# Kernel optimization log

Hardware: AMD Instinct MI355X
Metric: run time of the kernel (lower is better)

Reference implementation:

```python
import jax, jax.numpy as jnp
import numpy as np

D_MODEL = 1024
NUM_HEADS = 16
HEAD_DIM = D_MODEL // NUM_HEADS


def setup_inputs() -> dict:
    key = jax.random.key(0)
    ks = jax.random.split(key, 5)
    s = 1.0 / np.sqrt(D_MODEL)
    return {
        "x": jax.random.normal(ks[0], (4, 2048, D_MODEL), dtype=jnp.float32),
        "w_qkv": jax.random.uniform(ks[1], (3 * D_MODEL, D_MODEL), jnp.float32, -s, s),
        "b_qkv": jax.random.uniform(ks[2], (3 * D_MODEL,), jnp.float32, -s, s),
        "w_out": jax.random.uniform(ks[3], (D_MODEL, D_MODEL), jnp.float32, -s, s),
        "b_out": jax.random.uniform(ks[4], (D_MODEL,), jnp.float32, -s, s),
    }


def reference(x, w_qkv, b_qkv, w_out, b_out):
    B, T, D = x.shape
    # torch Linear: y = x @ W^T + b
    qkv = x @ w_qkv.T + b_qkv                                  # [B,T,3D]
    qkv = qkv.reshape(B, T, 3, NUM_HEADS, HEAD_DIM)
    q, k, v = jnp.moveaxis(qkv, 2, 0)                          # each [B,T,H,Hd]
    q = q.transpose(0, 2, 1, 3)                                # [B,H,T,Hd]
    k = k.transpose(0, 2, 1, 3)
    v = v.transpose(0, 2, 1, 3)
    scale = 1.0 / np.sqrt(HEAD_DIM).astype(np.float32)
    scores = jnp.einsum("bhqd,bhkd->bhqk", q, k) * scale       # [B,H,T,T]
    attn = jax.nn.softmax(scores, axis=-1)
    out = jnp.einsum("bhqk,bhkd->bhqd", attn, v)               # [B,H,T,Hd]
    out = out.transpose(0, 2, 1, 3).reshape(B, T, D)
    return out @ w_out.T + b_out
```

## Files before the change

### kernel.cpp

```cpp
#include <hip/hip_runtime.h>
#include <hip/hip_bf16.h>

#define SEQLEN  2048
#define DMODEL  1024
#define NHEADS  16
#define BT_ROWS 8192

typedef __attribute__((ext_vector_type(8))) _Float16 half8;
typedef __attribute__((ext_vector_type(4))) _Float16 half4;
typedef __attribute__((ext_vector_type(2))) _Float16 half2v;
typedef __attribute__((ext_vector_type(4))) float f32x4;
typedef unsigned short u16;

#define MFMAH(A, B, C)  __builtin_amdgcn_mfma_f32_16x16x32_f16((A), (B), (C), 0, 0, 0)

static __device__ __forceinline__ float fast_exp2(float x) {
#if __has_builtin(__builtin_amdgcn_exp2f)
    return __builtin_amdgcn_exp2f(x);
#else
    return exp2f(x);
#endif
}

typedef const __attribute__((address_space(1))) unsigned int* gas_t;
typedef __attribute__((address_space(3))) unsigned int* las_t;
static __device__ __forceinline__ void gld16(const void* g, void* l) {
    __builtin_amdgcn_global_load_lds((gas_t)g, (las_t)l, 16, 0, 0);
}

static __device__ __forceinline__ unsigned pack_f16x2(float a, float b) {
    return __builtin_bit_cast(unsigned, __builtin_amdgcn_cvt_pkrtz(a, b));
}

__global__ __launch_bounds__(256)
void cvt_f16(const float* __restrict__ in, u16* __restrict__ outp, int n4)
{
    int i = blockIdx.x * 256 + threadIdx.x;
    const int stride = gridDim.x * 256;
    for (; i < n4; i += stride) {
        const float4 v = ((const float4*)in)[i];
        const float f[4] = {v.x, v.y, v.z, v.w};
        ushort4 h4;
        u16 hh[4];
#pragma unroll
        for (int j = 0; j < 4; ++j)
            hh[j] = __builtin_bit_cast(u16, (_Float16)f[j]);
        h4.x = hh[0]; h4.y = hh[1]; h4.z = hh[2]; h4.w = hh[3];
        *(ushort4*)(outp + (size_t)i * 4) = h4;
    }
}

template<int MODE>
__global__ __launch_bounds__(256)
void gemm_nt_mfma(const u16* __restrict__ Af, const u16* __restrict__ Bf,
                  const float* __restrict__ bias, float* __restrict__ Cf,
                  u16* __restrict__ Pq, u16* __restrict__ Pk,
                  u16* __restrict__ Pv)
{
    __shared__ _Float16 Ah[128 * 32];
    __shared__ _Float16 Bh[128 * 32];

    const int tid  = threadIdx.x;
    const int lane = tid & 63;
    const int w    = tid >> 6;
    const int l15  = lane & 15;
    const int lg   = lane >> 4;
    const int wm   = w & 1;
    const int wn   = w >> 1;
    const int rowBase = blockIdx.y * 128;
    const int colBase = blockIdx.x * 128;

    const int srow = lane >> 2;
    const int sc   = lane & 3;

    f32x4 acc[4][4];
#pragma unroll
    for (int m = 0; m < 4; ++m)
#pragma unroll
        for (int n = 0; n < 4; ++n) acc[m][n] = (f32x4){0.f, 0.f, 0.f, 0.f};

    auto stage = [&](int kt) {
        const int k0 = kt * 32;
#pragma unroll
        for (int i = 0; i < 2; ++i) {
            const int slab = w * 2 + i;
            const int row  = slab * 16 + srow;
            const int gc   = sc ^ ((row >> 1) & 3);
            const size_t aoff = (size_t)(rowBase + row) * 1024 + k0 + gc * 8;
            const size_t boff = (size_t)(colBase + row) * 1024 + k0 + gc * 8;
            gld16(Af + aoff, &Ah[slab * 512]);
            gld16(Bf + boff, &Bh[slab * 512]);
        }
    };

    stage(0);

    for (int kt = 0; kt < 32; ++kt) {
        __syncthreads();

        half8 afh[4], bfh[4];
#pragma unroll
        for (int m = 0; m < 4; ++m) {
            const int row = wm * 64 + m * 16 + l15;
            const int cR  = lg ^ ((row >> 1) & 3);
            afh[m] = *(const half8*)&Ah[row * 32 + cR * 8];
        }
#pragma unroll
        for (int n = 0; n < 4; ++n) {
            const int row = wn * 64 + n * 16 + l15;
            const int cR  = lg ^ ((row >> 1) & 3);
            bfh[n] = *(const half8*)&Bh[row * 32 + cR * 8];
        }

        __syncthreads();
        if (kt < 31) stage(kt + 1);

        __builtin_amdgcn_s_setprio(1);
#pragma unroll
        for (int m = 0; m < 4; ++m)
#pragma unroll
            for (int n = 0; n < 4; ++n)
                acc[m][n] = MFMAH(afh[m], bfh[n], acc[m][n]);
        __builtin_amdgcn_s_setprio(0);
    }

    float bv[4];
#pragma unroll
    for (int n = 0; n < 4; ++n)
        bv[n] = bias[colBase + wn * 64 + n * 16 + l15];

    if constexpr (MODE == 0) {
#pragma unroll
        for (int m = 0; m < 4; ++m)
#pragma unroll
            for (int n = 0; n < 4; ++n) {
                const int col = colBase + wn * 64 + n * 16 + l15;
#pragma unroll
                for (int r = 0; r < 4; ++r) {
                    const int row = rowBase + wm * 64 + m * 16 + lg * 4 + r;
                    Cf[(size_t)row * 1024 + col] = acc[m][n][r] + bv[n];
                }
            }
    } else {
        const int comp = colBase >> 10;
        const float scale = (comp == 0) ? (0.125f * 1.44269504f) : 1.0f;
        u16* hp = (comp == 0) ? Pq : ((comp == 1) ? Pk : Pv);
        const int colc0 = colBase & 1023;
#pragma unroll
        for (int m = 0; m < 4; ++m)
#pragma unroll
            for (int n = 0; n < 4; ++n) {
                const int col = colc0 + wn * 64 + n * 16 + l15;
#pragma unroll
                for (int r = 0; r < 4; ++r) {
                    const int row = rowBase + wm * 64 + m * 16 + lg * 4 + r;
                    const float v = (acc[m][n][r] + bv[n]) * scale;
                    hp[(size_t)row * 1024 + col] =
                        __builtin_bit_cast(u16, (_Float16)v);
                }
            }
    }
}

__global__ __launch_bounds__(256, 4)
void flash_attn_mfma(const u16* __restrict__ Qf, const u16* __restrict__ Kf,
                     const u16* __restrict__ Vf, u16* __restrict__ Of)
{
    __shared__ __align__(16) _Float16 Kh[64 * 64];
    __shared__ __align__(16) _Float16 Vt[64][72];
    __shared__ __align__(16) _Float16 Pl[4][32][72];

    const int tid  = threadIdx.x;
    const int lane = tid & 63;
    const int w    = tid >> 6;
    const int l15  = lane & 15;
    const int lg   = lane >> 4;

    const int raw = blockIdx.x;
    const int swz = (raw & 7) * 128 + (raw >> 3);
    const int bh  = swz >> 4;
    const int qb  = swz & 15;
    const int b   = bh >> 4;
    const int h   = bh & 15;

    const int qRow0 = b * SEQLEN + qb * 128;
    const int kRowB = b * SEQLEN;
    const int hc    = h * 64;

    half8 Qr[2][2];
#pragma unroll
    for (int qt = 0; qt < 2; ++qt)
#pragma unroll
        for (int g = 0; g < 2; ++g) {
            const size_t off = (size_t)(qRow0 + w * 32 + qt * 16 + l15) * 1024
                             + hc + g * 32 + lg * 8;
            Qr[qt][g] = *(const half8*)(Qf + off);
        }

    f32x4 O[2][4];
    f32x4 accL[2];
#pragma unroll
    for (int qt = 0; qt < 2; ++qt) {
        accL[qt] = (f32x4){0.f, 0.f, 0.f, 0.f};
#pragma unroll
        for (int dt = 0; dt < 4; ++dt) O[qt][dt] = (f32x4){0.f, 0.f, 0.f, 0.f};
    }
    half8 vones;
#pragma unroll
    for (int j = 0; j < 8; ++j) vones[j] = (_Float16)1.0f;

    const int vp  = tid & 31;
    const int kv0 = (vp & 15) | ((vp >> 4) << 5);
    const int pcol = (kv0 & 15) * 4 + (kv0 >> 4);
    const int d0  = (tid >> 5) * 8;

    half8 kreg[2], vreg0, vreg1;
    int krow[2], kcc[2];

    auto load_tile = [&](int kt) {
#pragma unroll
        for (int i = 0; i < 2; ++i) {
            const int s = tid + 256 * i;
            const int row = s >> 3;
            const int c   = s & 7;
            krow[i] = row; kcc[i] = c;
            const int gc = c ^ (row & 7);
            const size_t g = (size_t)(kRowB + kt * 64 + row) * 1024 + hc + gc * 8;
            kreg[i] = *(const half8*)(Kf + g);
        }
        const size_t g = (size_t)(kRowB + kt * 64 + kv0) * 1024 + hc + d0;
        vreg0 = *(const half8*)(Vf + g);
        vreg1 = *(const half8*)(Vf + g + (size_t)16 * 1024);
    };

    load_tile(0);

    for (int kt = 0; kt < SEQLEN / 64; ++kt) {
        __syncthreads();
#pragma unroll
        for (int i = 0; i < 2; ++i)
            *(half8*)&Kh[krow[i] * 64 + kcc[i] * 8] = kreg[i];
#pragma unroll
        for (int j = 0; j < 8; ++j) {
            half2v pv;
            pv[0] = vreg0[j]; pv[1] = vreg1[j];
            *(half2v*)&Vt[d0 + j][pcol] = pv;
        }
        __syncthreads();

        if (kt < SEQLEN / 64 - 1) load_tile(kt + 1);

        f32x4 S[2][4];
#pragma unroll
        for (int qt = 0; qt < 2; ++qt)
#pragma unroll
            for (int k4 = 0; k4 < 4; ++k4) S[qt][k4] = (f32x4){0.f, 0.f, 0.f, 0.f};

        __builtin_amdgcn_s_setprio(1);
#pragma unroll
        for (int k4 = 0; k4 < 4; ++k4) {
            const int row = k4 * 16 + l15;
            const int swk = row & 7;
            const half8 kf0 = *(const half8*)&Kh[row * 64 + ((lg     ^ swk) * 8)];
            const half8 kf1 = *(const half8*)&Kh[row * 64 + (((4+lg) ^ swk) * 8)];
#pragma unroll
            for (int qt = 0; qt < 2; ++qt) {
                f32x4 a = S[qt][k4];
                a = MFMAH(Qr[qt][0], kf0, a);
                a = MFMAH(Qr[qt][1], kf1, a);
                S[qt][k4] = a;
            }
        }
        __builtin_amdgcn_s_setprio(0);

#pragma unroll
        for (int qt = 0; qt < 2; ++qt) {
#pragma unroll
            for (int r = 0; r < 4; ++r) {
                const float p0 = fast_exp2(S[qt][0][r]);
                const float p1 = fast_exp2(S[qt][1][r]);
                const float p2 = fast_exp2(S[qt][2][r]);
                const float p3 = fast_exp2(S[qt][3][r]);
                uint2 pw;
                pw.x = pack_f16x2(p0, p1);
                pw.y = pack_f16x2(p2, p3);
                *(uint2*)&Pl[w][qt * 16 + lg * 4 + r][l15 * 4] = pw;
            }
        }

        asm volatile("s_waitcnt lgkmcnt(0)" ::: "memory");
        __builtin_amdgcn_sched_barrier(0);

        __builtin_amdgcn_s_setprio(1);
#pragma unroll
        for (int ks = 0; ks < 2; ++ks) {
            half8 Pf[2];
#pragma unroll
            for (int qt = 0; qt < 2; ++qt)
                Pf[qt] = *(const half8*)&Pl[w][qt * 16 + l15][ks * 32 + lg * 8];
#pragma unroll
            for (int dt = 0; dt < 4; ++dt) {
                const half8 Vfr = *(const half8*)&Vt[dt * 16 + l15][ks * 32 + lg * 8];
#pragma unroll
                for (int qt = 0; qt < 2; ++qt)
                    O[qt][dt] = MFMAH(Pf[qt], Vfr, O[qt][dt]);
            }
#pragma unroll
            for (int qt = 0; qt < 2; ++qt)
                accL[qt] = MFMAH(Pf[qt], vones, accL[qt]);
        }
        __builtin_amdgcn_s_setprio(0);
    }

#pragma unroll
    for (int qt = 0; qt < 2; ++qt)
#pragma unroll
        for (int r = 0; r < 4; ++r) {
            const float inv = 1.0f / accL[qt][r];
            const int row = qRow0 + w * 32 + qt * 16 + lg * 4 + r;
#pragma unroll
            for (int dt = 0; dt < 4; ++dt) {
                const float o = O[qt][dt][r] * inv;
                const size_t off = (size_t)row * 1024 + hc + dt * 16 + l15;
                Of[off] = __builtin_bit_cast(u16, (_Float16)o);
            }
        }
}

extern "C" void kernel_launch(void* const* d_in, const int* in_sizes, int n_in,
                              void* d_out, int out_size, void* d_ws, size_t ws_size,
                              hipStream_t stream)
{
    const float* x     = (const float*)d_in[0];
    const float* w_qkv = (const float*)d_in[1];
    const float* b_qkv = (const float*)d_in[2];
    const float* w_out = (const float*)d_in[3];
    const float* b_out = (const float*)d_in[4];
    float* out = (float*)d_out;

    const size_t PLANE = (size_t)BT_ROWS * DMODEL;
    u16* Qf  = (u16*)d_ws;
    u16* Kf  = Qf + PLANE;
    u16* Vf  = Kf + PLANE;
    u16* xF  = Vf + PLANE;
    u16* aF  = xF;
    u16* wqkvF = xF + PLANE;
    u16* woutF = wqkvF + (size_t)3072 * 1024;

    cvt_f16<<<2048, 256, 0, stream>>>(x, xF, (int)(PLANE / 4));
    cvt_f16<<<768, 256, 0, stream>>>(w_qkv, wqkvF, 3072 * 1024 / 4);
    cvt_f16<<<256, 256, 0, stream>>>(w_out, woutF, 1024 * 1024 / 4);

    gemm_nt_mfma<1><<<dim3(3072 / 128, BT_ROWS / 128), 256, 0, stream>>>(
        xF, wqkvF, b_qkv, nullptr, Qf, Kf, Vf);

    flash_attn_mfma<<<dim3(1024), 256, 0, stream>>>(Qf, Kf, Vf, aF);

    gemm_nt_mfma<0><<<dim3(DMODEL / 128, BT_ROWS / 128), 256, 0, stream>>>(
        aF, woutF, b_out, out, nullptr, nullptr, nullptr);
}
```

Before: 205.6 us.

## Double query rows per attention block to reuse each K/V tile more

```diff
diff --git a/kernel.cpp b/kernel.cpp
--- a/kernel.cpp
+++ b/kernel.cpp
@@ -162,13 +162,13 @@
     }
 }
 
-__global__ __launch_bounds__(256, 4)
+__global__ __launch_bounds__(256, 2)
 void flash_attn_mfma(const u16* __restrict__ Qf, const u16* __restrict__ Kf,
                      const u16* __restrict__ Vf, u16* __restrict__ Of)
 {
     __shared__ __align__(16) _Float16 Kh[64 * 64];
     __shared__ __align__(16) _Float16 Vt[64][72];
-    __shared__ __align__(16) _Float16 Pl[4][32][72];
+    __shared__ __align__(16) _Float16 Pl[4][64][72];
 
     const int tid  = threadIdx.x;
     const int lane = tid & 63;
@@ -177,30 +177,30 @@
     const int lg   = lane >> 4;
 
     const int raw = blockIdx.x;
-    const int swz = (raw & 7) * 128 + (raw >> 3);
-    const int bh  = swz >> 4;
-    const int qb  = swz & 15;
+    const int swz = (raw & 7) * 64 + (raw >> 3);
+    const int bh  = swz >> 3;
+    const int qb  = swz & 7;
     const int b   = bh >> 4;
     const int h   = bh & 15;
 
-    const int qRow0 = b * SEQLEN + qb * 128;
+    const int qRow0 = b * SEQLEN + qb * 256 + w * 64;
     const int kRowB = b * SEQLEN;
     const int hc    = h * 64;
 
-    half8 Qr[2][2];
-#pragma unroll
-    for (int qt = 0; qt < 2; ++qt)
+    half8 Qr[4][2];
+#pragma unroll
+    for (int qt = 0; qt < 4; ++qt)
 #pragma unroll
         for (int g = 0; g < 2; ++g) {
-            const size_t off = (size_t)(qRow0 + w * 32 + qt * 16 + l15) * 1024
+            const size_t off = (size_t)(qRow0 + qt * 16 + l15) * 1024
                              + hc + g * 32 + lg * 8;
             Qr[qt][g] = *(const half8*)(Qf + off);
         }
 
-    f32x4 O[2][4];
-    f32x4 accL[2];
-#pragma unroll
-    for (int qt = 0; qt < 2; ++qt) {
+    f32x4 O[4][4];
+    f32x4 accL[4];
+#pragma unroll
+    for (int qt = 0; qt < 4; ++qt) {
         accL[qt] = (f32x4){0.f, 0.f, 0.f, 0.f};
 #pragma unroll
         for (int dt = 0; dt < 4; ++dt) O[qt][dt] = (f32x4){0.f, 0.f, 0.f, 0.f};
@@ -250,37 +250,35 @@
 
         if (kt < SEQLEN / 64 - 1) load_tile(kt + 1);
 
-        f32x4 S[2][4];
-#pragma unroll
-        for (int qt = 0; qt < 2; ++qt)
-#pragma unroll
-            for (int k4 = 0; k4 < 4; ++k4) S[qt][k4] = (f32x4){0.f, 0.f, 0.f, 0.f};
-
-        __builtin_amdgcn_s_setprio(1);
+        half8 kf[4][2];
 #pragma unroll
         for (int k4 = 0; k4 < 4; ++k4) {
             const int row = k4 * 16 + l15;
             const int swk = row & 7;
-            const half8 kf0 = *(const half8*)&Kh[row * 64 + ((lg     ^ swk) * 8)];
-            const half8 kf1 = *(const half8*)&Kh[row * 64 + (((4+lg) ^ swk) * 8)];
-#pragma unroll
-            for (int qt = 0; qt < 2; ++qt) {
-                f32x4 a = S[qt][k4];
-                a = MFMAH(Qr[qt][0], kf0, a);
-                a = MFMAH(Qr[qt][1], kf1, a);
-                S[qt][k4] = a;
-            }
-        }
-        __builtin_amdgcn_s_setprio(0);
-
-#pragma unroll
-        for (int qt = 0; qt < 2; ++qt) {
+            kf[k4][0] = *(const half8*)&Kh[row * 64 + ((lg     ^ swk) * 8)];
+            kf[k4][1] = *(const half8*)&Kh[row * 64 + (((4+lg) ^ swk) * 8)];
+        }
+
+#pragma unroll
+        for (int qt = 0; qt < 4; ++qt) {
+            f32x4 S[4];
+#pragma unroll
+            for (int k4 = 0; k4 < 4; ++k4) S[k4] = (f32x4){0.f, 0.f, 0.f, 0.f};
+
+            __builtin_amdgcn_s_setprio(1);
+#pragma unroll
+            for (int k4 = 0; k4 < 4; ++k4) {
+                S[k4] = MFMAH(Qr[qt][0], kf[k4][0], S[k4]);
+                S[k4] = MFMAH(Qr[qt][1], kf[k4][1], S[k4]);
+            }
+            __builtin_amdgcn_s_setprio(0);
+
 #pragma unroll
             for (int r = 0; r < 4; ++r) {
-                const float p0 = fast_exp2(S[qt][0][r]);
-                const float p1 = fast_exp2(S[qt][1][r]);
-                const float p2 = fast_exp2(S[qt][2][r]);
-                const float p3 = fast_exp2(S[qt][3][r]);
+                const float p0 = fast_exp2(S[0][r]);
+                const float p1 = fast_exp2(S[1][r]);
+                const float p2 = fast_exp2(S[2][r]);
+                const float p3 = fast_exp2(S[3][r]);
                 uint2 pw;
                 pw.x = pack_f16x2(p0, p1);
                 pw.y = pack_f16x2(p2, p3);
@@ -294,30 +292,30 @@
         __builtin_amdgcn_s_setprio(1);
 #pragma unroll
         for (int ks = 0; ks < 2; ++ks) {
-            half8 Pf[2];
-#pragma unroll
-            for (int qt = 0; qt < 2; ++qt)
+            half8 Pf[4];
+#pragma unroll
+            for (int qt = 0; qt < 4; ++qt)
                 Pf[qt] = *(const half8*)&Pl[w][qt * 16 + l15][ks * 32 + lg * 8];
 #pragma unroll
             for (int dt = 0; dt < 4; ++dt) {
                 const half8 Vfr = *(const half8*)&Vt[dt * 16 + l15][ks * 32 + lg * 8];
 #pragma unroll
-                for (int qt = 0; qt < 2; ++qt)
+                for (int qt = 0; qt < 4; ++qt)
                     O[qt][dt] = MFMAH(Pf[qt], Vfr, O[qt][dt]);
             }
 #pragma unroll
-            for (int qt = 0; qt < 2; ++qt)
+            for (int qt = 0; qt < 4; ++qt)
                 accL[qt] = MFMAH(Pf[qt], vones, accL[qt]);
         }
         __builtin_amdgcn_s_setprio(0);
     }
 
 #pragma unroll
-    for (int qt = 0; qt < 2; ++qt)
+    for (int qt = 0; qt < 4; ++qt)
 #pragma unroll
         for (int r = 0; r < 4; ++r) {
             const float inv = 1.0f / accL[qt][r];
-            const int row = qRow0 + w * 32 + qt * 16 + lg * 4 + r;
+            const int row = qRow0 + qt * 16 + lg * 4 + r;
 #pragma unroll
             for (int dt = 0; dt < 4; ++dt) {
                 const float o = O[qt][dt][r] * inv;
@@ -354,7 +352,7 @@
     gemm_nt_mfma<1><<<dim3(3072 / 128, BT_ROWS / 128), 256, 0, stream>>>(
         xF, wqkvF, b_qkv, nullptr, Qf, Kf, Vf);
 
-    flash_attn_mfma<<<dim3(1024), 256, 0, stream>>>(Qf, Kf, Vf, aF);
+    flash_attn_mfma<<<dim3(512), 256, 0, stream>>>(Qf, Kf, Vf, aF);
 
     gemm_nt_mfma<0><<<dim3(DMODEL / 128, BT_ROWS / 128), 256, 0, stream>>>(
         aF, woutF, b_out, out, nullptr, nullptr, nullptr);
```

Result: faster. 196.4 us (-4.5%).
